# Optimization experiments

Hardware: AMD Instinct MI355X
Metric: run time of the kernel (lower is better)

Reference implementation:

```python
import jax, jax.numpy as jnp
import numpy as np

N_NODES = 50000
N_EDGES = 1200000
D_FEAT = 64
HIDDEN = 32


def setup_inputs() -> dict:
    key = jax.random.key(0)
    ks = jax.random.split(key, 9)
    x = jax.random.normal(ks[0], (N_NODES, D_FEAT), dtype=jnp.float32)
    edge_index = jax.random.randint(ks[1], (2, N_EDGES), 0, N_NODES, dtype=jnp.int64)
    u = jax.random.normal(ks[2], (N_NODES,), dtype=jnp.float32)
    d_in = 2 * D_FEAT
    # MLP: Linear(d_in,H) -> relu -> Linear(H,H) -> relu -> Linear(H,1)
    W1 = jax.random.normal(ks[3], (d_in, HIDDEN), dtype=jnp.float32) / np.sqrt(d_in)
    b1 = jnp.zeros((HIDDEN,), dtype=jnp.float32)
    W2 = jax.random.normal(ks[4], (HIDDEN, HIDDEN), dtype=jnp.float32) / np.sqrt(HIDDEN)
    b2 = jnp.zeros((HIDDEN,), dtype=jnp.float32)
    W3 = jax.random.normal(ks[5], (HIDDEN, 1), dtype=jnp.float32) / np.sqrt(HIDDEN)
    b3 = jnp.zeros((1,), dtype=jnp.float32)
    return {"x": x, "edge_index": edge_index, "u": u,
            "W1": W1, "b1": b1, "W2": W2, "b2": b2, "W3": W3, "b3": b3}


def reference(x, edge_index, u, W1, b1, W2, b2, W3, b3):
    row, col = edge_index[0], edge_index[1]
    # gather + concat: [E, 2*D]
    x_edge = jnp.concatenate([x[row], x[col]], axis=-1)
    # per-edge MLP -> scalar weight per edge
    h = jax.nn.relu(x_edge @ W1 + b1)
    h = jax.nn.relu(h @ W2 + b2)
    edge_weight = (h @ W3 + b3)[:, 0]  # [E]
    # spmm: f[i] = sum_{e: row[e]==i} w_e * u[col[e]]
    f = jax.ops.segment_sum(edge_weight * u[col], row, num_segments=x.shape[0])
    return f
```

## Files before the change

kernel.cpp:

```cpp
#include <hip/hip_runtime.h>

#define N_NODES 50000
#define N_EDGES 1200000
#define N_TILES (N_NODES / 16)
#define W1T_STRIDE 72
#define K1_BLOCKS 782

#define N_BUCKETS 196
#define BUCKET_CAP 7168
#define EDGES_PER_BLOCK 1920
#define KA_BLOCKS 625
#define D1_BLOCKS (K1_BLOCKS + KA_BLOCKS)
#define KB_SPLIT 4

typedef __attribute__((ext_vector_type(8))) short short8;
typedef __attribute__((ext_vector_type(4))) float floatx4;

__device__ __forceinline__ unsigned short f32_to_bf16(float f) {
    unsigned int v = __float_as_uint(f);
    unsigned int r = v + 0x7FFFu + ((v >> 16) & 1u);
    return (unsigned short)(r >> 16);
}
__device__ __forceinline__ float bf16_to_f32(unsigned short s) {
    return __uint_as_float(((unsigned int)s) << 16);
}
__device__ __forceinline__ unsigned int pack_bf16x2(float lo, float hi) {
    return (unsigned int)f32_to_bf16(lo) | ((unsigned int)f32_to_bf16(hi) << 16);
}

__global__ __launch_bounds__(256) void fused_pre_bin(
    const float* __restrict__ x, const float* __restrict__ W1,
    const float* __restrict__ b1,
    const int* __restrict__ row, const int* __restrict__ col,
    unsigned short* __restrict__ P1, unsigned short* __restrict__ P2,
    unsigned int* __restrict__ buf, int* __restrict__ cursor,
    float* __restrict__ out)
{
    __shared__ union {
        unsigned short W1t[64 * W1T_STRIDE];
        struct {
            unsigned short rankv[EDGES_PER_BLOCK];
            int hist[N_BUCKETS];
            int base[N_BUCKETS];
        } bin;
    } sh;

    const int tid = threadIdx.x;
    const int bid = blockIdx.x;

    if (bid < K1_BLOCKS) {
        const int gtid = bid * 256 + tid;
        for (int i = gtid; i < N_NODES; i += K1_BLOCKS * 256)
            out[i] = 0.0f;

        for (int e = tid; e < 128 * 32; e += 256) {
            const int kp = e >> 5, jp = e & 31;
            sh.W1t[((kp < 64) ? jp : jp + 32) * W1T_STRIDE + (kp & 63)] =
                f32_to_bf16(W1[e]);
        }
        __syncthreads();

        const int lane = tid & 63;
        const int n = lane & 15;
        const int q = lane >> 4;

        const int tile = bid * 4 + (tid >> 6);
        if (tile >= N_TILES) return;

        short8 bw[4][2];
        #pragma unroll
        for (int G = 0; G < 4; ++G)
            #pragma unroll
            for (int h = 0; h < 2; ++h)
                bw[G][h] = *(const short8*)
                    &sh.W1t[(n + 16 * G) * W1T_STRIDE + h * 32 + q * 8];
        const float bias0 = b1[n], bias1 = b1[n + 16];

        const int node = tile * 16 + n;
        const float4* xp  = (const float4*)(x + (size_t)node * 64 + q * 8);
        const float4 xa = xp[0], xb = xp[1];
        const float4* xp2 = (const float4*)(x + (size_t)node * 64 + 32 + q * 8);
        const float4 xc = xp2[0], xd = xp2[1];

        short8 a0, a1;
        a0[0] = (short)f32_to_bf16(xa.x); a0[1] = (short)f32_to_bf16(xa.y);
        a0[2] = (short)f32_to_bf16(xa.z); a0[3] = (short)f32_to_bf16(xa.w);
        a0[4] = (short)f32_to_bf16(xb.x); a0[5] = (short)f32_to_bf16(xb.y);
        a0[6] = (short)f32_to_bf16(xb.z); a0[7] = (short)f32_to_bf16(xb.w);
        a1[0] = (short)f32_to_bf16(xc.x); a1[1] = (short)f32_to_bf16(xc.y);
        a1[2] = (short)f32_to_bf16(xc.z); a1[3] = (short)f32_to_bf16(xc.w);
        a1[4] = (short)f32_to_bf16(xd.x); a1[5] = (short)f32_to_bf16(xd.y);
        a1[6] = (short)f32_to_bf16(xd.z); a1[7] = (short)f32_to_bf16(xd.w);

        floatx4 acc[4];
        #pragma unroll
        for (int G = 0; G < 4; ++G) {
            const float bi = (G == 0) ? bias0 : (G == 1) ? bias1 : 0.0f;
            acc[G] = (floatx4){bi, bi, bi, bi};
            acc[G] = __builtin_amdgcn_mfma_f32_16x16x32_bf16(a0, bw[G][0], acc[G], 0, 0, 0);
            acc[G] = __builtin_amdgcn_mfma_f32_16x16x32_bf16(a1, bw[G][1], acc[G], 0, 0, 0);
        }
        unsigned int* P1d = (unsigned int*)P1;
        unsigned int* P2d = (unsigned int*)P2;
        #pragma unroll
        for (int r = 0; r < 4; ++r) {
            const int nr = tile * 16 + q * 4 + r;
            P1d[(size_t)nr * 16 + n] = pack_bf16x2(acc[0][r], acc[1][r]);
            P2d[(size_t)nr * 16 + n] = pack_bf16x2(acc[2][r], acc[3][r]);
        }
    } else {
        for (int b = tid; b < N_BUCKETS; b += 256) sh.bin.hist[b] = 0;
        __syncthreads();

        const int blockStart = (bid - K1_BLOCKS) * EDGES_PER_BLOCK;

        for (int i = tid; i < EDGES_PER_BLOCK; i += 256) {
            const int r = row[blockStart + i];
            sh.bin.rankv[i] = (unsigned short)atomicAdd(&sh.bin.hist[r >> 8], 1);
        }
        __syncthreads();

        for (int b = tid; b < N_BUCKETS; b += 256)
            sh.bin.base[b] = atomicAdd(&cursor[b], sh.bin.hist[b]);
        __syncthreads();

        for (int i = tid; i < EDGES_PER_BLOCK; i += 256) {
            const int r = row[blockStart + i];
            const int c = col[blockStart + i];
            const int bin = r >> 8;
            buf[(size_t)bin * BUCKET_CAP + sh.bin.base[bin] + (int)sh.bin.rankv[i]] =
                ((unsigned int)(r & 255) << 24) | (unsigned int)c;
        }
    }
}

__global__ __launch_bounds__(512) void bucket_mlp(
    const float* __restrict__ u,
    const float* __restrict__ W2, const float* __restrict__ b2,
    const float* __restrict__ W3, const float* __restrict__ b3,
    const unsigned short* __restrict__ P1, const unsigned short* __restrict__ P2,
    const unsigned int* __restrict__ buf, const int* __restrict__ cursor,
    float* __restrict__ out)
{
    __shared__ float accs[256];
    const int tid = threadIdx.x;
    if (tid < 256) accs[tid] = 0.0f;

    const int b = blockIdx.x >> 2;
    const int s = blockIdx.x & (KB_SPLIT - 1);

    const int lane = tid & 63;
    const int n = lane & 15;
    const int q = lane >> 4;
    const int wave = tid >> 6;

    short8 bf0, bf1;
    #pragma unroll
    for (int i = 0; i < 8; ++i) {
        const int F = q * 4 + (i >> 1) + 16 * (i & 1);
        bf0[i] = (short)f32_to_bf16(W2[F * 32 + n]);
        bf1[i] = (short)f32_to_bf16(W2[F * 32 + n + 16]);
    }
    const float w3n0 = W3[n], w3n1 = W3[n + 16];
    const float b2n0 = b2[n], b2n1 = b2[n + 16];
    const float bias3 = b3[0];

    __syncthreads();

    const int cnt = cursor[b];
    const unsigned int* bb = buf + (size_t)b * BUCKET_CAP;
    const unsigned short* P1b = P1 + (size_t)b * 256 * 32;
    const int nch = (cnt + 31) >> 5;

    #pragma unroll 1
    for (int ch = s * 8 + wave; ch < nch; ch += KB_SPLIT * 8) {
        const int base0 = ch * 32;

        int rl[2], cI[2];
        #pragma unroll
        for (int t = 0; t < 2; ++t) {
            int e = base0 + t * 16 + n;
            if (e >= cnt) e = cnt - 1;
            const unsigned int ent = bb[e];
            rl[t] = (int)(ent >> 24);
            cI[t] = (int)(ent & 0x1FFFFu);
        }
        int r2 = 0; float u2 = 0.0f;
        if (n < 8) {
            const int eloc = base0 + 16 * (n >> 2) + 4 * q + (n & 3);
            const unsigned int ent2 = bb[(eloc < cnt) ? eloc : 0];
            r2 = (int)(ent2 >> 24);
            u2 = (eloc < cnt) ? u[ent2 & 0x1FFFFu] : 0.0f;
        }
        short8 v1[2], v2[2];
        #pragma unroll
        for (int t = 0; t < 2; ++t) {
            v1[t] = *(const short8*)(P1b + (size_t)rl[t] * 32 + q * 8);
            v2[t] = *(const short8*)(P2 + (size_t)cI[t] * 32 + q * 8);
        }

        float tr[2][4];
        #pragma unroll
        for (int t = 0; t < 2; ++t) {
            short8 a;
            #pragma unroll
            for (int i = 0; i < 8; ++i) {
                const float f1 = bf16_to_f32((unsigned short)v1[t][i]);
                const float f2 = bf16_to_f32((unsigned short)v2[t][i]);
                a[i] = (short)f32_to_bf16(fmaxf(f1 + f2, 0.0f));
            }
            floatx4 d0 = {b2n0, b2n0, b2n0, b2n0};
            floatx4 d1 = {b2n1, b2n1, b2n1, b2n1};
            d0 = __builtin_amdgcn_mfma_f32_16x16x32_bf16(a, bf0, d0, 0, 0, 0);
            d1 = __builtin_amdgcn_mfma_f32_16x16x32_bf16(a, bf1, d1, 0, 0, 0);
            #pragma unroll
            for (int r = 0; r < 4; ++r)
                tr[t][r] = fmaxf(d0[r], 0.0f) * w3n0 + fmaxf(d1[r], 0.0f) * w3n1;
        }

        #pragma unroll
        for (int mask = 1; mask < 16; mask <<= 1) {
            #pragma unroll
            for (int t = 0; t < 2; ++t)
                #pragma unroll
                for (int r = 0; r < 4; ++r)
                    tr[t][r] += __shfl_xor(tr[t][r], mask, 64);
        }

        if (n < 8) {
            const float va0 = (n & 4) ? tr[1][0] : tr[0][0];
            const float va1 = (n & 4) ? tr[1][1] : tr[0][1];
            const float va2 = (n & 4) ? tr[1][2] : tr[0][2];
            const float va3 = (n & 4) ? tr[1][3] : tr[0][3];
            const float vb0 = (n & 2) ? va2 : va0;
            const float vb1 = (n & 2) ? va3 : va1;
            const float v   = (n & 1) ? vb1 : vb0;
            atomicAdd(&accs[r2], (v + bias3) * u2);
        }
    }

    __syncthreads();

    if (tid < 256) {
        const int node = b * 256 + tid;
        if (node < N_NODES) atomicAdd(out + node, accs[tid]);
    }
}

extern "C" void kernel_launch(void* const* d_in, const int* in_sizes, int n_in,
                              void* d_out, int out_size, void* d_ws, size_t ws_size,
                              hipStream_t stream)
{
    const float* x    = (const float*)d_in[0];
    const int*   eidx = (const int*)  d_in[1];
    const float* u    = (const float*)d_in[2];
    const float* W1   = (const float*)d_in[3];
    const float* b1   = (const float*)d_in[4];
    const float* W2   = (const float*)d_in[5];
    const float* b2   = (const float*)d_in[6];
    const float* W3   = (const float*)d_in[7];
    const float* b3   = (const float*)d_in[8];

    const int* row = eidx;
    const int* col = eidx + N_EDGES;

    unsigned short* P1 = (unsigned short*)d_ws;
    unsigned short* P2 = (unsigned short*)((char*)d_ws + (size_t)N_NODES * 64);
    unsigned int*  buf = (unsigned int*)((char*)d_ws + (size_t)N_NODES * 128);
    int* cursor = (int*)((char*)d_ws + (size_t)N_NODES * 128
                         + (size_t)N_BUCKETS * BUCKET_CAP * 4);
    float* out = (float*)d_out;

    hipMemsetAsync(cursor, 0, N_BUCKETS * sizeof(int), stream);

    fused_pre_bin<<<D1_BLOCKS, 256, 0, stream>>>(
        x, W1, b1, row, col, P1, P2, buf, cursor, out);

    bucket_mlp<<<N_BUCKETS * KB_SPLIT, 512, 0, stream>>>(
        u, W2, b2, W3, b3, P1, P2, buf, cursor, out);
}
```

Before: 133.8 us.

## Software-pipeline bucket MLP gathers and enlarge binning blocks

The bucket_mlp loop is restructured into a two-stage software pipeline: bucket entries are prefetched two chunks ahead and the P1/P2/u gathers one chunk ahead, so gather latency overlaps the MFMA compute. The bf16 add/relu/convert is rewritten to work on packed 32-bit words and uses the packed __float22bfloat162_rn conversion. The binning kernel also gets fewer, larger blocks (9600 edges each), which cuts global cursor atomics but lowers parallelism in that phase. The prefetching raises register pressure, which may reduce occupancy.

Result: slower. 137.9 us (+3.0%).

```diff
diff --git a/kernel.cpp b/kernel.cpp
--- a/kernel.cpp
+++ b/kernel.cpp
@@ -1,4 +1,5 @@
 #include <hip/hip_runtime.h>
+#include <hip/hip_bf16.h>
 
 #define N_NODES 50000
 #define N_EDGES 1200000
@@ -8,8 +9,8 @@
 
 #define N_BUCKETS 196
 #define BUCKET_CAP 7168
-#define EDGES_PER_BLOCK 1920
-#define KA_BLOCKS 625
+#define EDGES_PER_BLOCK 9600
+#define KA_BLOCKS 125
 #define D1_BLOCKS (K1_BLOCKS + KA_BLOCKS)
 #define KB_SPLIT 4
 
@@ -20,9 +21,6 @@
     unsigned int v = __float_as_uint(f);
     unsigned int r = v + 0x7FFFu + ((v >> 16) & 1u);
     return (unsigned short)(r >> 16);
-}
-__device__ __forceinline__ float bf16_to_f32(unsigned short s) {
-    return __uint_as_float(((unsigned int)s) << 16);
 }
 __device__ __forceinline__ unsigned int pack_bf16x2(float lo, float hi) {
     return (unsigned int)f32_to_bf16(lo) | ((unsigned int)f32_to_bf16(hi) << 16);
@@ -134,6 +132,17 @@
     }
 }
 
+struct EntS {
+    unsigned int g0, g1;
+    unsigned int o;
+    int ov;
+};
+struct GatS {
+    short8 v1a, v2a, v1b, v2b;
+    float u2;
+    int r2;
+};
+
 __global__ __launch_bounds__(512) void bucket_mlp(
     const float* __restrict__ u,
     const float* __restrict__ W2, const float* __restrict__ b2,
@@ -172,43 +181,52 @@
     const unsigned short* P1b = P1 + (size_t)b * 256 * 32;
     const int nch = (cnt + 31) >> 5;
 
-    #pragma unroll 1
-    for (int ch = s * 8 + wave; ch < nch; ch += KB_SPLIT * 8) {
+    auto load_ent = [&](int ch) -> EntS {
+        EntS E;
         const int base0 = ch * 32;
-
-        int rl[2], cI[2];
-        #pragma unroll
-        for (int t = 0; t < 2; ++t) {
-            int e = base0 + t * 16 + n;
-            if (e >= cnt) e = cnt - 1;
-            const unsigned int ent = bb[e];
-            rl[t] = (int)(ent >> 24);
-            cI[t] = (int)(ent & 0x1FFFFu);
-        }
-        int r2 = 0; float u2 = 0.0f;
+        int e0 = base0 + n;        if (e0 >= cnt) e0 = cnt - 1;
+        int e1 = base0 + 16 + n;   if (e1 >= cnt) e1 = cnt - 1;
+        E.g0 = bb[e0];
+        E.g1 = bb[e1];
+        E.o = 0u; E.ov = 0;
         if (n < 8) {
             const int eloc = base0 + 16 * (n >> 2) + 4 * q + (n & 3);
-            const unsigned int ent2 = bb[(eloc < cnt) ? eloc : 0];
-            r2 = (int)(ent2 >> 24);
-            u2 = (eloc < cnt) ? u[ent2 & 0x1FFFFu] : 0.0f;
-        }
-        short8 v1[2], v2[2];
+            E.ov = (eloc < cnt);
+            E.o = bb[E.ov ? eloc : 0];
+        }
+        return E;
+    };
+    auto load_gat = [&](const EntS& E) -> GatS {
+        GatS G;
+        G.v1a = *(const short8*)(P1b + (size_t)(E.g0 >> 24) * 32 + q * 8);
+        G.v2a = *(const short8*)(P2  + (size_t)(E.g0 & 0x1FFFFu) * 32 + q * 8);
+        G.v1b = *(const short8*)(P1b + (size_t)(E.g1 >> 24) * 32 + q * 8);
+        G.v2b = *(const short8*)(P2  + (size_t)(E.g1 & 0x1FFFFu) * 32 + q * 8);
+        G.r2 = (int)(E.o >> 24);
+        G.u2 = E.ov ? u[E.o & 0x1FFFFu] : 0.0f;
+        return G;
+    };
+    auto compute = [&](const GatS& G) {
+        float tr[2][4];
         #pragma unroll
         for (int t = 0; t < 2; ++t) {
-            v1[t] = *(const short8*)(P1b + (size_t)rl[t] * 32 + q * 8);
-            v2[t] = *(const short8*)(P2 + (size_t)cI[t] * 32 + q * 8);
-        }
-
-        float tr[2][4];
-        #pragma unroll
-        for (int t = 0; t < 2; ++t) {
-            short8 a;
+            const short8 v1 = t ? G.v1b : G.v1a;
+            const short8 v2 = t ? G.v2b : G.v2a;
+            union VU { short8 s; unsigned int w[4]; };
+            VU x1, x2, ar;
+            x1.s = v1; x2.s = v2;
             #pragma unroll
-            for (int i = 0; i < 8; ++i) {
-                const float f1 = bf16_to_f32((unsigned short)v1[t][i]);
-                const float f2 = bf16_to_f32((unsigned short)v2[t][i]);
-                a[i] = (short)f32_to_bf16(fmaxf(f1 + f2, 0.0f));
+            for (int i = 0; i < 4; ++i) {
+                const unsigned int w1 = x1.w[i], w2 = x2.w[i];
+                float lo = __uint_as_float(w1 << 16) + __uint_as_float(w2 << 16);
+                float hi = __uint_as_float(w1 & 0xFFFF0000u) + __uint_as_float(w2 & 0xFFFF0000u);
+                lo = fmaxf(lo, 0.0f);
+                hi = fmaxf(hi, 0.0f);
+                union { __hip_bfloat162 h; unsigned int u32; } cv;
+                cv.h = __float22bfloat162_rn(make_float2(lo, hi));
+                ar.w[i] = cv.u32;
             }
+            const short8 a = ar.s;
             floatx4 d0 = {b2n0, b2n0, b2n0, b2n0};
             floatx4 d1 = {b2n1, b2n1, b2n1, b2n1};
             d0 = __builtin_amdgcn_mfma_f32_16x16x32_bf16(a, bf0, d0, 0, 0, 0);
@@ -235,7 +253,25 @@
             const float vb0 = (n & 2) ? va2 : va0;
             const float vb1 = (n & 2) ? va3 : va1;
             const float v   = (n & 1) ? vb1 : vb0;
-            atomicAdd(&accs[r2], (v + bias3) * u2);
+            atomicAdd(&accs[G.r2], (v + bias3) * G.u2);
+        }
+    };
+
+    int c0 = s * 8 + wave;
+    if (c0 < nch) {
+        int c1 = c0 + 32;
+        EntS eCur = load_ent(c0);
+        EntS eNxt = (c1 < nch) ? load_ent(c1) : eCur;
+        GatS gCur = load_gat(eCur);
+        for (;;) {
+            const int c2 = c1 + 32;
+            EntS eN2  = (c2 < nch) ? load_ent(c2) : eNxt;
+            GatS gNxt = (c1 < nch) ? load_gat(eNxt) : gCur;
+            compute(gCur);
+            if (c1 >= nch) break;
+            c1 = c2;
+            eNxt = eN2;
+            gCur = gNxt;
         }
     }
 
```

## Merge binning, node GEMM and bucket MLP into one cooperative persistent kernel

Applied to the files above, without the earlier changes.

Replaces the memset plus two launches with a single cooperative kernel of 512 persistent blocks. Grid-wide syncs separate the cursor reset, the binning/GEMM phase and the bucket MLP phase, and work is assigned through grid-stride task loops. Binning tasks become larger (4800 edges) and the bucket split is doubled with 256-thread blocks, which changes the task granularity. The aim is to remove launch and memset overhead and the idle tail between kernels, at the cost of grid.sync latency and lower parallelism per phase. If the cooperative launch fails, it falls back to two regular launches.

Result: slower. 259.7 us (+94.0%).

```diff
diff --git a/kernel.cpp b/kernel.cpp
--- a/kernel.cpp
+++ b/kernel.cpp
@@ -1,17 +1,22 @@
 #include <hip/hip_runtime.h>
+#include <hip/hip_cooperative_groups.h>
+
+namespace cg = cooperative_groups;
 
 #define N_NODES 50000
 #define N_EDGES 1200000
 #define N_TILES (N_NODES / 16)
 #define W1T_STRIDE 72
-#define K1_BLOCKS 782
 
 #define N_BUCKETS 196
 #define BUCKET_CAP 7168
-#define EDGES_PER_BLOCK 1920
-#define KA_BLOCKS 625
-#define D1_BLOCKS (K1_BLOCKS + KA_BLOCKS)
-#define KB_SPLIT 4
+#define EDGES_PER_BLOCK 4800
+#define KA_BLOCKS 250
+#define GEMM_BLOCKS 782
+#define A1_TASKS (KA_BLOCKS + GEMM_BLOCKS)
+#define KB_SPLIT 8
+#define KB_TASKS (N_BUCKETS * KB_SPLIT)
+#define COOP_GRID 512
 
 typedef __attribute__((ext_vector_type(8))) short short8;
 typedef __attribute__((ext_vector_type(4))) float floatx4;
@@ -28,13 +33,16 @@
     return (unsigned int)f32_to_bf16(lo) | ((unsigned int)f32_to_bf16(hi) << 16);
 }
 
-__global__ __launch_bounds__(256) void fused_pre_bin(
+__global__ __launch_bounds__(256, 4) void edgemlp_all(
     const float* __restrict__ x, const float* __restrict__ W1,
     const float* __restrict__ b1,
     const int* __restrict__ row, const int* __restrict__ col,
+    const float* __restrict__ u,
+    const float* __restrict__ W2, const float* __restrict__ b2,
+    const float* __restrict__ W3, const float* __restrict__ b3,
     unsigned short* __restrict__ P1, unsigned short* __restrict__ P2,
     unsigned int* __restrict__ buf, int* __restrict__ cursor,
-    float* __restrict__ out)
+    float* __restrict__ out, int mode)
 {
     __shared__ union {
         unsigned short W1t[64 * W1T_STRIDE];
@@ -43,116 +51,114 @@
             int hist[N_BUCKETS];
             int base[N_BUCKETS];
         } bin;
+        float accs[256];
     } sh;
+
+    cg::grid_group grid = cg::this_grid();
 
     const int tid = threadIdx.x;
     const int bid = blockIdx.x;
-
-    if (bid < K1_BLOCKS) {
-        const int gtid = bid * 256 + tid;
-        for (int i = gtid; i < N_NODES; i += K1_BLOCKS * 256)
-            out[i] = 0.0f;
-
-        for (int e = tid; e < 128 * 32; e += 256) {
-            const int kp = e >> 5, jp = e & 31;
-            sh.W1t[((kp < 64) ? jp : jp + 32) * W1T_STRIDE + (kp & 63)] =
-                f32_to_bf16(W1[e]);
-        }
-        __syncthreads();
-
-        const int lane = tid & 63;
-        const int n = lane & 15;
-        const int q = lane >> 4;
-
-        const int tile = bid * 4 + (tid >> 6);
-        if (tile >= N_TILES) return;
-
-        short8 bw[4][2];
-        #pragma unroll
-        for (int G = 0; G < 4; ++G)
-            #pragma unroll
-            for (int h = 0; h < 2; ++h)
-                bw[G][h] = *(const short8*)
-                    &sh.W1t[(n + 16 * G) * W1T_STRIDE + h * 32 + q * 8];
-        const float bias0 = b1[n], bias1 = b1[n + 16];
-
-        const int node = tile * 16 + n;
-        const float4* xp  = (const float4*)(x + (size_t)node * 64 + q * 8);
-        const float4 xa = xp[0], xb = xp[1];
-        const float4* xp2 = (const float4*)(x + (size_t)node * 64 + 32 + q * 8);
-        const float4 xc = xp2[0], xd = xp2[1];
-
-        short8 a0, a1;
-        a0[0] = (short)f32_to_bf16(xa.x); a0[1] = (short)f32_to_bf16(xa.y);
-        a0[2] = (short)f32_to_bf16(xa.z); a0[3] = (short)f32_to_bf16(xa.w);
-        a0[4] = (short)f32_to_bf16(xb.x); a0[5] = (short)f32_to_bf16(xb.y);
-        a0[6] = (short)f32_to_bf16(xb.z); a0[7] = (short)f32_to_bf16(xb.w);
-        a1[0] = (short)f32_to_bf16(xc.x); a1[1] = (short)f32_to_bf16(xc.y);
-        a1[2] = (short)f32_to_bf16(xc.z); a1[3] = (short)f32_to_bf16(xc.w);
-        a1[4] = (short)f32_to_bf16(xd.x); a1[5] = (short)f32_to_bf16(xd.y);
-        a1[6] = (short)f32_to_bf16(xd.z); a1[7] = (short)f32_to_bf16(xd.w);
-
-        floatx4 acc[4];
-        #pragma unroll
-        for (int G = 0; G < 4; ++G) {
-            const float bi = (G == 0) ? bias0 : (G == 1) ? bias1 : 0.0f;
-            acc[G] = (floatx4){bi, bi, bi, bi};
-            acc[G] = __builtin_amdgcn_mfma_f32_16x16x32_bf16(a0, bw[G][0], acc[G], 0, 0, 0);
-            acc[G] = __builtin_amdgcn_mfma_f32_16x16x32_bf16(a1, bw[G][1], acc[G], 0, 0, 0);
-        }
-        unsigned int* P1d = (unsigned int*)P1;
-        unsigned int* P2d = (unsigned int*)P2;
-        #pragma unroll
-        for (int r = 0; r < 4; ++r) {
-            const int nr = tile * 16 + q * 4 + r;
-            P1d[(size_t)nr * 16 + n] = pack_bf16x2(acc[0][r], acc[1][r]);
-            P2d[(size_t)nr * 16 + n] = pack_bf16x2(acc[2][r], acc[3][r]);
-        }
-    } else {
-        for (int b = tid; b < N_BUCKETS; b += 256) sh.bin.hist[b] = 0;
-        __syncthreads();
-
-        const int blockStart = (bid - K1_BLOCKS) * EDGES_PER_BLOCK;
-
-        for (int i = tid; i < EDGES_PER_BLOCK; i += 256) {
-            const int r = row[blockStart + i];
-            sh.bin.rankv[i] = (unsigned short)atomicAdd(&sh.bin.hist[r >> 8], 1);
-        }
-        __syncthreads();
-
-        for (int b = tid; b < N_BUCKETS; b += 256)
-            sh.bin.base[b] = atomicAdd(&cursor[b], sh.bin.hist[b]);
-        __syncthreads();
-
-        for (int i = tid; i < EDGES_PER_BLOCK; i += 256) {
-            const int r = row[blockStart + i];
-            const int c = col[blockStart + i];
-            const int bin = r >> 8;
-            buf[(size_t)bin * BUCKET_CAP + sh.bin.base[bin] + (int)sh.bin.rankv[i]] =
-                ((unsigned int)(r & 255) << 24) | (unsigned int)c;
-        }
-    }
-}
-
-__global__ __launch_bounds__(512) void bucket_mlp(
-    const float* __restrict__ u,
-    const float* __restrict__ W2, const float* __restrict__ b2,
-    const float* __restrict__ W3, const float* __restrict__ b3,
-    const unsigned short* __restrict__ P1, const unsigned short* __restrict__ P2,
-    const unsigned int* __restrict__ buf, const int* __restrict__ cursor,
-    float* __restrict__ out)
-{
-    __shared__ float accs[256];
-    const int tid = threadIdx.x;
-    if (tid < 256) accs[tid] = 0.0f;
-
-    const int b = blockIdx.x >> 2;
-    const int s = blockIdx.x & (KB_SPLIT - 1);
+    const int gstride = (int)gridDim.x;
+    const int gtid = bid * 256 + tid;
 
     const int lane = tid & 63;
     const int n = lane & 15;
     const int q = lane >> 4;
     const int wave = tid >> 6;
+    const bool coop = (mode == 0);
+
+    if (mode <= 1) {
+        for (int i = gtid; i < N_NODES; i += gstride * 256) out[i] = 0.0f;
+        if (coop) {
+            if (gtid < N_BUCKETS) cursor[gtid] = 0;
+            grid.sync();
+        }
+
+        for (int task = bid; task < A1_TASKS; task += gstride) {
+            if (task < KA_BLOCKS) {
+                for (int b = tid; b < N_BUCKETS; b += 256) sh.bin.hist[b] = 0;
+                __syncthreads();
+
+                const int blockStart = task * EDGES_PER_BLOCK;
+
+                for (int i = tid; i < EDGES_PER_BLOCK; i += 256) {
+                    const int r = row[blockStart + i];
+                    sh.bin.rankv[i] =
+                        (unsigned short)atomicAdd(&sh.bin.hist[r >> 8], 1);
+                }
+                __syncthreads();
+
+                for (int b = tid; b < N_BUCKETS; b += 256)
+                    sh.bin.base[b] = atomicAdd(&cursor[b], sh.bin.hist[b]);
+                __syncthreads();
+
+                for (int i = tid; i < EDGES_PER_BLOCK; i += 256) {
+                    const int r = row[blockStart + i];
+                    const int c = col[blockStart + i];
+                    const int bin = r >> 8;
+                    buf[(size_t)bin * BUCKET_CAP + sh.bin.base[bin]
+                        + (int)sh.bin.rankv[i]] =
+                        ((unsigned int)(r & 255) << 24) | (unsigned int)c;
+                }
+            } else {
+                for (int e = tid; e < 128 * 32; e += 256) {
+                    const int kp = e >> 5, jp = e & 31;
+                    sh.W1t[((kp < 64) ? jp : jp + 32) * W1T_STRIDE + (kp & 63)] =
+                        f32_to_bf16(W1[e]);
+                }
+                __syncthreads();
+
+                const int tile = (task - KA_BLOCKS) * 4 + wave;
+                if (tile < N_TILES) {
+                    short8 bw[4][2];
+                    #pragma unroll
+                    for (int G = 0; G < 4; ++G)
+                        #pragma unroll
+                        for (int h = 0; h < 2; ++h)
+                            bw[G][h] = *(const short8*)
+                                &sh.W1t[(n + 16 * G) * W1T_STRIDE + h * 32 + q * 8];
+                    const float bias0 = b1[n], bias1 = b1[n + 16];
+
+                    const int node = tile * 16 + n;
+                    const float4* xp  = (const float4*)(x + (size_t)node * 64 + q * 8);
+                    const float4 xa = xp[0], xb = xp[1];
+                    const float4* xp2 = (const float4*)(x + (size_t)node * 64 + 32 + q * 8);
+                    const float4 xc = xp2[0], xd = xp2[1];
+
+                    short8 a0, a1;
+                    a0[0] = (short)f32_to_bf16(xa.x); a0[1] = (short)f32_to_bf16(xa.y);
+                    a0[2] = (short)f32_to_bf16(xa.z); a0[3] = (short)f32_to_bf16(xa.w);
+                    a0[4] = (short)f32_to_bf16(xb.x); a0[5] = (short)f32_to_bf16(xb.y);
+                    a0[6] = (short)f32_to_bf16(xb.z); a0[7] = (short)f32_to_bf16(xb.w);
+                    a1[0] = (short)f32_to_bf16(xc.x); a1[1] = (short)f32_to_bf16(xc.y);
+                    a1[2] = (short)f32_to_bf16(xc.z); a1[3] = (short)f32_to_bf16(xc.w);
+                    a1[4] = (short)f32_to_bf16(xd.x); a1[5] = (short)f32_to_bf16(xd.y);
+                    a1[6] = (short)f32_to_bf16(xd.z); a1[7] = (short)f32_to_bf16(xd.w);
+
+                    floatx4 acc[4];
+                    #pragma unroll
+                    for (int G = 0; G < 4; ++G) {
+                        const float bi = (G == 0) ? bias0 : (G == 1) ? bias1 : 0.0f;
+                        acc[G] = (floatx4){bi, bi, bi, bi};
+                        acc[G] = __builtin_amdgcn_mfma_f32_16x16x32_bf16(a0, bw[G][0], acc[G], 0, 0, 0);
+                        acc[G] = __builtin_amdgcn_mfma_f32_16x16x32_bf16(a1, bw[G][1], acc[G], 0, 0, 0);
+                    }
+                    unsigned int* P1d = (unsigned int*)P1;
+                    unsigned int* P2d = (unsigned int*)P2;
+                    #pragma unroll
+                    for (int r = 0; r < 4; ++r) {
+                        const int nr = tile * 16 + q * 4 + r;
+                        P1d[(size_t)nr * 16 + n] = pack_bf16x2(acc[0][r], acc[1][r]);
+                        P2d[(size_t)nr * 16 + n] = pack_bf16x2(acc[2][r], acc[3][r]);
+                    }
+                }
+            }
+            __syncthreads();
+        }
+    }
+
+    if (coop) grid.sync();
+    if (mode == 1) return;
 
     short8 bf0, bf1;
     #pragma unroll
@@ -165,85 +171,90 @@
     const float b2n0 = b2[n], b2n1 = b2[n + 16];
     const float bias3 = b3[0];
 
-    __syncthreads();
-
-    const int cnt = cursor[b];
-    const unsigned int* bb = buf + (size_t)b * BUCKET_CAP;
-    const unsigned short* P1b = P1 + (size_t)b * 256 * 32;
-    const int nch = (cnt + 31) >> 5;
-
-    #pragma unroll 1
-    for (int ch = s * 8 + wave; ch < nch; ch += KB_SPLIT * 8) {
-        const int base0 = ch * 32;
-
-        int rl[2], cI[2];
-        #pragma unroll
-        for (int t = 0; t < 2; ++t) {
-            int e = base0 + t * 16 + n;
-            if (e >= cnt) e = cnt - 1;
-            const unsigned int ent = bb[e];
-            rl[t] = (int)(ent >> 24);
-            cI[t] = (int)(ent & 0x1FFFFu);
-        }
-        int r2 = 0; float u2 = 0.0f;
-        if (n < 8) {
-            const int eloc = base0 + 16 * (n >> 2) + 4 * q + (n & 3);
-            const unsigned int ent2 = bb[(eloc < cnt) ? eloc : 0];
-            r2 = (int)(ent2 >> 24);
-            u2 = (eloc < cnt) ? u[ent2 & 0x1FFFFu] : 0.0f;
-        }
-        short8 v1[2], v2[2];
-        #pragma unroll
-        for (int t = 0; t < 2; ++t) {
-            v1[t] = *(const short8*)(P1b + (size_t)rl[t] * 32 + q * 8);
-            v2[t] = *(const short8*)(P2 + (size_t)cI[t] * 32 + q * 8);
-        }
-
-        float tr[2][4];
-        #pragma unroll
-        for (int t = 0; t < 2; ++t) {
-            short8 a;
+    for (int task = bid; task < KB_TASKS; task += gstride) {
+        const int b = task >> 3;
+        const int s = task & (KB_SPLIT - 1);
+
+        sh.accs[tid] = 0.0f;
+        __syncthreads();
+
+        const int cnt = cursor[b];
+        const unsigned int* bb = buf + (size_t)b * BUCKET_CAP;
+        const unsigned short* P1b = P1 + (size_t)b * 256 * 32;
+        const int nch = (cnt + 31) >> 5;
+
+        #pragma unroll 1
+        for (int ch = s * 4 + wave; ch < nch; ch += 32) {
+            const int base0 = ch * 32;
+
+            int rl[2], cI[2];
             #pragma unroll
-            for (int i = 0; i < 8; ++i) {
-                const float f1 = bf16_to_f32((unsigned short)v1[t][i]);
-                const float f2 = bf16_to_f32((unsigned short)v2[t][i]);
-                a[i] = (short)f32_to_bf16(fmaxf(f1 + f2, 0.0f));
-            }
-            floatx4 d0 = {b2n0, b2n0, b2n0, b2n0};
-            floatx4 d1 = {b2n1, b2n1, b2n1, b2n1};
-            d0 = __builtin_amdgcn_mfma_f32_16x16x32_bf16(a, bf0, d0, 0, 0, 0);
-            d1 = __builtin_amdgcn_mfma_f32_16x16x32_bf16(a, bf1, d1, 0, 0, 0);
+            for (int t = 0; t < 2; ++t) {
+                int e = base0 + t * 16 + n;
+                if (e >= cnt) e = cnt - 1;
+                const unsigned int ent = bb[e];
+                rl[t] = (int)(ent >> 24);
+                cI[t] = (int)(ent & 0x1FFFFu);
+            }
+            int r2 = 0; float u2 = 0.0f;
+            if (n < 8) {
+                const int eloc = base0 + 16 * (n >> 2) + 4 * q + (n & 3);
+                const unsigned int ent2 = bb[(eloc < cnt) ? eloc : 0];
+                r2 = (int)(ent2 >> 24);
+                u2 = (eloc < cnt) ? u[ent2 & 0x1FFFFu] : 0.0f;
+            }
+            short8 v1[2], v2[2];
             #pragma unroll
-            for (int r = 0; r < 4; ++r)
-                tr[t][r] = fmaxf(d0[r], 0.0f) * w3n0 + fmaxf(d1[r], 0.0f) * w3n1;
-        }
-
-        #pragma unroll
-        for (int mask = 1; mask < 16; mask <<= 1) {
+            for (int t = 0; t < 2; ++t) {
+                v1[t] = *(const short8*)(P1b + (size_t)rl[t] * 32 + q * 8);
+                v2[t] = *(const short8*)(P2 + (size_t)cI[t] * 32 + q * 8);
+            }
+
+            float tr[2][4];
             #pragma unroll
-            for (int t = 0; t < 2; ++t)
+            for (int t = 0; t < 2; ++t) {
+                short8 a;
+                #pragma unroll
+                for (int i = 0; i < 8; ++i) {
+                    const float f1 = bf16_to_f32((unsigned short)v1[t][i]);
+                    const float f2 = bf16_to_f32((unsigned short)v2[t][i]);
+                    a[i] = (short)f32_to_bf16(fmaxf(f1 + f2, 0.0f));
+                }
+                floatx4 d0 = {b2n0, b2n0, b2n0, b2n0};
+                floatx4 d1 = {b2n1, b2n1, b2n1, b2n1};
+                d0 = __builtin_amdgcn_mfma_f32_16x16x32_bf16(a, bf0, d0, 0, 0, 0);
+                d1 = __builtin_amdgcn_mfma_f32_16x16x32_bf16(a, bf1, d1, 0, 0, 0);
                 #pragma unroll
                 for (int r = 0; r < 4; ++r)
-                    tr[t][r] += __shfl_xor(tr[t][r], mask, 64);
+                    tr[t][r] = fmaxf(d0[r], 0.0f) * w3n0 + fmaxf(d1[r], 0.0f) * w3n1;
+            }
+
+            #pragma unroll
+            for (int mask = 1; mask < 16; mask <<= 1) {
+                #pragma unroll
+                for (int t = 0; t < 2; ++t)
+                    #pragma unroll
+                    for (int r = 0; r < 4; ++r)
+                        tr[t][r] += __shfl_xor(tr[t][r], mask, 64);
+            }
+
+            if (n < 8) {
+                const float va0 = (n & 4) ? tr[1][0] : tr[0][0];
+                const float va1 = (n & 4) ? tr[1][1] : tr[0][1];
+                const float va2 = (n & 4) ? tr[1][2] : tr[0][2];
+                const float va3 = (n & 4) ? tr[1][3] : tr[0][3];
+                const float vb0 = (n & 2) ? va2 : va0;
+                const float vb1 = (n & 2) ? va3 : va1;
+                const float v   = (n & 1) ? vb1 : vb0;
+                atomicAdd(&sh.accs[r2], (v + bias3) * u2);
+            }
         }
 
-        if (n < 8) {
-            const float va0 = (n & 4) ? tr[1][0] : tr[0][0];
-            const float va1 = (n & 4) ? tr[1][1] : tr[0][1];
-            const float va2 = (n & 4) ? tr[1][2] : tr[0][2];
-            const float va3 = (n & 4) ? tr[1][3] : tr[0][3];
-            const float vb0 = (n & 2) ? va2 : va0;
-            const float vb1 = (n & 2) ? va3 : va1;
-            const float v   = (n & 1) ? vb1 : vb0;
-            atomicAdd(&accs[r2], (v + bias3) * u2);
-        }
-    }
-
-    __syncthreads();
-
-    if (tid < 256) {
+        __syncthreads();
+
         const int node = b * 256 + tid;
-        if (node < N_NODES) atomicAdd(out + node, accs[tid]);
+        if (node < N_NODES) atomicAdd(out + node, sh.accs[tid]);
+        __syncthreads();
     }
 }
 
@@ -271,11 +282,24 @@
                          + (size_t)N_BUCKETS * BUCKET_CAP * 4);
     float* out = (float*)d_out;
 
-    hipMemsetAsync(cursor, 0, N_BUCKETS * sizeof(int), stream);
-
-    fused_pre_bin<<<D1_BLOCKS, 256, 0, stream>>>(
-        x, W1, b1, row, col, P1, P2, buf, cursor, out);
-
-    bucket_mlp<<<N_BUCKETS * KB_SPLIT, 512, 0, stream>>>(
-        u, W2, b2, W3, b3, P1, P2, buf, cursor, out);
-}
+    int mode0 = 0;
+    void* args[] = {
+        (void*)&x, (void*)&W1, (void*)&b1, (void*)&row, (void*)&col,
+        (void*)&u, (void*)&W2, (void*)&b2, (void*)&W3, (void*)&b3,
+        (void*)&P1, (void*)&P2, (void*)&buf, (void*)&cursor, (void*)&out,
+        (void*)&mode0
+    };
+    hipError_t err = hipLaunchCooperativeKernel(
+        (const void*)edgemlp_all, dim3(COOP_GRID), dim3(256), args, 0, stream);
+
+    if (err != hipSuccess) {
+        (void)hipGetLastError();
+        hipMemsetAsync(cursor, 0, N_BUCKETS * sizeof(int), stream);
+        edgemlp_all<<<A1_TASKS, 256, 0, stream>>>(
+            x, W1, b1, row, col, u, W2, b2, W3, b3,
+            P1, P2, buf, cursor, out, 1);
+        edgemlp_all<<<KB_TASKS, 256, 0, stream>>>(
+            x, W1, b1, row, col, u, W2, b2, W3, b3,
+            P1, P2, buf, cursor, out, 2);
+    }
+}
```
